# Kernel tuning notes

Measured on AMD Instinct MI355X. Metric: run time of the kernel, lower is better.

The kernel has to match this reference:

```python
import jax, jax.numpy as jnp
import numpy as np

TOL = 0.5          # Time_tolerance
DECAY = 1.0        # decay_rate
RES = 0.03         # integral_resolution
T_MAX = 120.0
G = 4000           # int(T_MAX / RES)


def setup_inputs() -> dict:
    key = jax.random.key(0)
    ks = jax.random.split(key, 8)
    B, N, H = 128, 64, 128
    times0 = jnp.sort(jax.random.uniform(ks[0], (B, N), dtype=jnp.float32) * T_MAX, axis=-1)
    times1 = jnp.sort(jax.random.uniform(ks[1], (B, N), dtype=jnp.float32) * T_MAX, axis=-1)
    states0 = jax.random.randint(ks[2], (B, N), 0, 2, dtype=jnp.int32)
    states1 = jax.random.randint(ks[3], (B, N), 0, 2, dtype=jnp.int32)
    head_times = jnp.sort(jax.random.uniform(ks[4], (B, H), dtype=jnp.float32) * T_MAX, axis=-1)
    head_states = jax.random.randint(ks[5], (B, H), 0, 2, dtype=jnp.int32)
    base = jnp.full((1,), -0.2, dtype=jnp.float32)  # torch.ones(1) * -0.2
    weights = jax.random.normal(ks[6], (2,), dtype=jnp.float32) * 0.1
    return dict(times0=times0, states0=states0, times1=times1, states1=states1,
                head_times=head_times, head_states=head_states, base=base, weights=weights)


def _intensity(t, times0, states0, times1, states1, head_times, head_states, base, wn):
    # t: [B,T] evaluation times; times*: [B,N]; head_*: [B,H]
    te = t[..., None]                                   # [B,T,1]
    t0 = times0[:, None, :]                             # [B,1,N]
    t1 = times1[:, None, :]
    s0 = states0[:, None, :]
    s1 = states1[:, None, :]
    # exp(-decay*(t - tau)); clamp dt>=0 so masked-out (future) events don't overflow
    dec0 = jnp.exp(-DECAY * jnp.maximum(te - t0, 0.0))  # [B,T,N]
    dec1 = jnp.exp(-DECAY * jnp.maximum(te - t1, 0.0))
    # Formula 0: body [0,1], signs [1,1], relations (0 BEFORE 1), (1 BEFORE head)
    A = jnp.where((t0 <= te) & (s0 == 1), dec0, 0.0)                 # history mask + kernel on pred0
    Bm = jnp.where((t1 < te - TOL) & (s1 == 1), dec1, 0.0)           # (t1 BEFORE head) + history mask
    M = (times0[:, :, None] - times1[:, None, :] < -TOL).astype(t.dtype)  # [B,N,N] (t0 BEFORE t1)
    feat0 = jnp.einsum('bti,bij,btj->bt', A, M, Bm)  # sum over itertools.product pairs
    # Formula 1: body [0], sign [0], relation (0 BEFORE head)
    feat1 = jnp.sum(jnp.where((t0 < te - TOL) & (s0 == 0), dec0, 0.0), axis=-1)
    # formula effect: cur_state via idx = sum(t > head_times) - 1 (numpy negative-index wrap)
    cnt = jnp.sum(te > head_times[:, None, :], axis=-1)              # [B,T]
    Hn = head_times.shape[-1]
    cur_state = jnp.take_along_axis(head_states, (cnt - 1) % Hn, axis=-1)
    eff0 = jnp.where(cur_state == 0, 1.0, -1.0).astype(t.dtype)      # head sign 1 -> +1 iff counter_state==1
    eff1 = -eff0                                                      # head sign 0
    return jnp.exp(base[0] + wn[0] * feat0 * eff0 + wn[1] * feat1 * eff1)


def reference(times0, states0, times1, states1, head_times, head_states, base, weights):
    wn = jax.nn.softmax(weights)  # exp(w)/sum exp(w)
    B = times0.shape[0]
    grid = jnp.broadcast_to((jnp.arange(G, dtype=times0.dtype) * RES)[None, :], (B, G))
    lam_grid = _intensity(grid, times0, states0, times1, states1, head_times, head_states, base, wn)
    lam_ev = _intensity(head_times[:, 1:], times0, states0, times1, states1, head_times, head_states, base, wn)
    log_sum = jnp.sum(jnp.log(lam_ev))
    integral = jnp.sum(lam_grid) * RES
    return (log_sum - integral).reshape(1)
```

## Files before the change

### kernel.cpp

```cpp
#include <hip/hip_runtime.h>
#include <math.h>

constexpr int Bb = 128;
constexpr int Nn = 64;
constexpr int Hh = 128;
constexpr int Gg = 4000;
constexpr float  TOLf = 0.5f;
constexpr double RESd = 0.03;

constexpr int GBLK  = 16;
constexpr int NGRID = Bb * GBLK;
constexpr int NBLK  = NGRID + Bb;
constexpr int TSTRIDE = 72;

__device__ __forceinline__ int lb64(const float* __restrict__ a, float key) {
    int lo = (a[31] < key) ? 32 : 0;
    lo += (a[lo + 15] < key) ? 16 : 0;
    lo += (a[lo + 7]  < key) ? 8  : 0;
    lo += (a[lo + 3]  < key) ? 4  : 0;
    lo += (a[lo + 1]  < key) ? 2  : 0;
    lo += (a[lo]      < key) ? 1  : 0;
    lo += (a[lo]      < key) ? 1  : 0;
    return lo;
}
__device__ __forceinline__ int ub64(const float* __restrict__ a, float key) {
    int lo = (a[31] <= key) ? 32 : 0;
    lo += (a[lo + 15] <= key) ? 16 : 0;
    lo += (a[lo + 7]  <= key) ? 8  : 0;
    lo += (a[lo + 3]  <= key) ? 4  : 0;
    lo += (a[lo + 1]  <= key) ? 2  : 0;
    lo += (a[lo]      <= key) ? 1  : 0;
    lo += (a[lo]      <= key) ? 1  : 0;
    return lo;
}
__device__ __forceinline__ int lb128(const float* __restrict__ a, float key) {
    int lo = (a[63] < key) ? 64 : 0;
    lo += (a[lo + 31] < key) ? 32 : 0;
    lo += (a[lo + 15] < key) ? 16 : 0;
    lo += (a[lo + 7]  < key) ? 8  : 0;
    lo += (a[lo + 3]  < key) ? 4  : 0;
    lo += (a[lo + 1]  < key) ? 2  : 0;
    lo += (a[lo]      < key) ? 1  : 0;
    lo += (a[lo]      < key) ? 1  : 0;
    return lo;
}

__global__ __launch_bounds__(64) void precompute_kernel(
    const float* __restrict__ times0, const int* __restrict__ states0,
    const float* __restrict__ times1, const int* __restrict__ states1,
    double* __restrict__ Ps_all, double* __restrict__ Qs_all,
    double* __restrict__ SW_all, double* __restrict__ SWP_all,
    int* __restrict__ kT_all)
{
    const int b = blockIdx.x;
    const int i = threadIdx.x;

    __shared__ float  t1s[Nn];
    __shared__ int    j0s[Nn];
    __shared__ double Ps_sh[Nn + 1];

    const float t0 = times0[b * Nn + i];
    const float t1 = times1[b * Nn + i];
    const int   s0 = states0[b * Nn + i];
    const int   s1 = states1[b * Nn + i];
    t1s[i] = t1;
    __syncthreads();

    int j0 = 0;
    #pragma unroll
    for (int j = 0; j < Nn; ++j)
        j0 += (t0 - t1s[j] >= -TOLf) ? 1 : 0;
    j0s[i] = j0;

    const double e0 = exp((double)t0);
    double vp = (s1 == 1) ? exp((double)t1) : 0.0;
    double vq = (s0 == 0) ? e0 : 0.0;
    const double W = (s0 == 1) ? e0 : 0.0;
    double vw = W;

    #pragma unroll
    for (int off = 1; off < 64; off <<= 1) {
        double op = __shfl_up(vp, off, 64);
        double oq = __shfl_up(vq, off, 64);
        double ow = __shfl_up(vw, off, 64);
        if (i >= off) { vp += op; vq += oq; vw += ow; }
    }
    Ps_sh[i + 1] = vp;
    if (i == 0) Ps_sh[0] = 0.0;
    __syncthreads();

    double vwp = W * Ps_sh[j0];
    #pragma unroll
    for (int off = 1; off < 64; off <<= 1) {
        double o = __shfl_up(vwp, off, 64);
        if (i >= off) vwp += o;
    }

    int kc = 0;
    #pragma unroll
    for (int j = 0; j < Nn; ++j)
        kc += (j0s[j] <= i) ? 1 : 0;

    double* Ps  = Ps_all  + b * TSTRIDE;
    double* Qs  = Qs_all  + b * TSTRIDE;
    double* SW  = SW_all  + b * TSTRIDE;
    double* SWP = SWP_all + b * TSTRIDE;
    int*    kT  = kT_all  + b * TSTRIDE;

    Ps[i + 1]  = vp;  Qs[i + 1]  = vq;
    SW[i + 1]  = vw;  SWP[i + 1] = vwp;
    kT[i] = kc;
    if (i == 0) {
        Ps[0] = 0.0; Qs[0] = 0.0; SW[0] = 0.0; SWP[0] = 0.0;
        kT[Nn] = Nn;
    }
}

__global__ __launch_bounds__(256) void eval_kernel(
    const float* __restrict__ times0, const float* __restrict__ times1,
    const float* __restrict__ head_times, const int* __restrict__ head_states,
    const float* __restrict__ base, const float* __restrict__ weights,
    const double* __restrict__ Ps_all, const double* __restrict__ Qs_all,
    const double* __restrict__ SW_all, const double* __restrict__ SWP_all,
    const int* __restrict__ kT_all,
    double* __restrict__ partials)
{
    __shared__ float  t0s[Nn], t1s[Nn];
    __shared__ float  hts[Hh];
    __shared__ int    hss[Hh];
    __shared__ double Ps[Nn + 1], Qs[Nn + 1], SW[Nn + 1], SWP[Nn + 1];
    __shared__ int    kT[Nn + 1];
    __shared__ double wsh[3];
    __shared__ double redsh[4];

    const int tid = threadIdx.x;
    const bool isEvent = blockIdx.x >= (unsigned)NGRID;
    const int b     = isEvent ? (blockIdx.x - NGRID) : (blockIdx.x >> 4);
    const int gbase = isEvent ? 0 : ((blockIdx.x & 15) << 8);
    const double tbase = (double)gbase * 0.03;

    if (tid < Nn) {
        t0s[tid] = times0[b * Nn + tid];
        t1s[tid] = times1[b * Nn + tid];
    } else if (tid < 192) {
        const int k = tid - 64;
        hts[k] = head_times[b * Hh + k];
        hss[k] = head_states[b * Hh + k];
    } else {
        const double sE = isEvent ? 1.0 : exp(-tbase);
        int k = tid - 192;
        const int base_i = b * TSTRIDE;
        Ps[k]  = Ps_all [base_i + k] * sE;
        Qs[k]  = Qs_all [base_i + k] * sE;
        SW[k]  = SW_all [base_i + k] * sE;
        SWP[k] = SWP_all[base_i + k] * (sE * sE);
        kT[k]  = kT_all [base_i + k];
        if (tid == 192) {
            k = Nn;
            Ps[k]  = Ps_all [base_i + k] * sE;
            Qs[k]  = Qs_all [base_i + k] * sE;
            SW[k]  = SW_all [base_i + k] * sE;
            SWP[k] = SWP_all[base_i + k] * (sE * sE);
            kT[k]  = kT_all [base_i + k];
        }
    }
    if (tid == 0) {
        const double w0 = (double)weights[0], w1 = (double)weights[1];
        const double mw = fmax(w0, w1);
        const double e0 = exp(w0 - mw), e1 = exp(w1 - mw);
        wsh[0] = e0 / (e0 + e1);
        wsh[1] = e1 / (e0 + e1);
        wsh[2] = (double)base[0];
    }
    __syncthreads();

    double contrib = 0.0;

    if (isEvent) {
        if (tid >= 1 && tid < Hh) {
            const float tf = hts[tid];
            const float thr = tf - TOLf;
            const int c   = lb64(t1s, thr);
            const int c0  = lb64(t0s, thr);
            const int c1  = ub64(t0s, tf);
            const int cnt = lb128(hts, tf);

            const int m = min(c1, kT[c]);
            const double a  = Ps[c] * SW[m] - SWP[m];
            const double ed = exp(-(double)tf);
            const double f0 = a * ed * ed;
            const double f1 = Qs[c0] * ed;
            const int cur = hss[((unsigned)(cnt - 1)) & (unsigned)(Hh - 1)];
            const double eff = (cur == 0) ? 1.0 : -1.0;
            contrib = wsh[2] + eff * (wsh[0] * f0 - wsh[1] * f1);
        }
    } else {
        const int g = gbase + tid;
        if (g < Gg) {
            const float tf = (float)g * 0.03f;
            const float thr = tf - TOLf;
            const int c   = lb64(t1s, thr);
            const int c0  = lb64(t0s, thr);
            const int c1  = ub64(t0s, tf);
            const int cnt = lb128(hts, tf);

            const int m = min(c1, kT[c]);
            const double a = Ps[c] * SW[m] - SWP[m];
            const double dt = (double)tf - tbase;
            const float f0 = (float)a * __expf((float)(-2.0 * dt));
            const float f1 = (float)Qs[c0] * __expf((float)(-dt));
            const int cur = hss[((unsigned)(cnt - 1)) & (unsigned)(Hh - 1)];
            const float eff = (cur == 0) ? 1.0f : -1.0f;
            const float ll = (float)wsh[2] + eff * ((float)wsh[0] * f0 - (float)wsh[1] * f1);
            contrib = -RESd * (double)__expf(ll);
        }
    }

    double v = contrib;
    #pragma unroll
    for (int off = 32; off > 0; off >>= 1) v += __shfl_down(v, off, 64);
    if ((tid & 63) == 0) redsh[tid >> 6] = v;
    __syncthreads();
    if (tid == 0) partials[blockIdx.x] = redsh[0] + redsh[1] + redsh[2] + redsh[3];
}

__global__ __launch_bounds__(256) void finalize_kernel(
    const double* __restrict__ partials, float* __restrict__ out)
{
    __shared__ double redsh[4];
    const int tid = threadIdx.x;
    double v = 0.0;
    for (int i = tid; i < NBLK; i += 256) v += partials[i];
    #pragma unroll
    for (int off = 32; off > 0; off >>= 1) v += __shfl_down(v, off, 64);
    if ((tid & 63) == 0) redsh[tid >> 6] = v;
    __syncthreads();
    if (tid == 0) out[0] = (float)(redsh[0] + redsh[1] + redsh[2] + redsh[3]);
}

extern "C" void kernel_launch(void* const* d_in, const int* in_sizes, int n_in,
                              void* d_out, int out_size, void* d_ws, size_t ws_size,
                              hipStream_t stream) {
    const float* times0      = (const float*)d_in[0];
    const int*   states0     = (const int*)  d_in[1];
    const float* times1      = (const float*)d_in[2];
    const int*   states1     = (const int*)  d_in[3];
    const float* head_times  = (const float*)d_in[4];
    const int*   head_states = (const int*)  d_in[5];
    const float* base        = (const float*)d_in[6];
    const float* weights     = (const float*)d_in[7];

    double* Ps_all  = (double*)d_ws;
    double* Qs_all  = Ps_all  + Bb * TSTRIDE;
    double* SW_all  = Qs_all  + Bb * TSTRIDE;
    double* SWP_all = SW_all  + Bb * TSTRIDE;
    int*    kT_all  = (int*)(SWP_all + Bb * TSTRIDE);
    double* partials = (double*)(kT_all + Bb * TSTRIDE);

    precompute_kernel<<<Bb, 64, 0, stream>>>(times0, states0, times1, states1,
                                             Ps_all, Qs_all, SW_all, SWP_all, kT_all);
    eval_kernel<<<NBLK, 256, 0, stream>>>(times0, times1, head_times, head_states,
                                          base, weights,
                                          Ps_all, Qs_all, SW_all, SWP_all, kT_all,
                                          partials);
    finalize_kernel<<<1, 256, 0, stream>>>(partials, (float*)d_out);
}
```

Measured before the change: 78.80 us.

## Precompute piecewise segment payloads so grid points use one merged-breakpoint search

The precompute kernel now merges all breakpoints per batch (shifted event thresholds and head times) into one sorted array of 512 entries. For each segment it stores a float4 payload with the pre-scaled feat0 and feat1 coefficients, sign and weights folded in. Each grid thread then does one 9-step binary search plus two exps instead of four binary searches and double-precision prefix-sum lookups. In exchange the precompute kernel does more serial work, and exact float threshold keys (thr_key via ulp stepping) are needed to keep the segment boundaries equivalent.

```diff
diff --git a/kernel.cpp b/kernel.cpp
--- a/kernel.cpp
+++ b/kernel.cpp
@@ -12,6 +12,11 @@
 constexpr int NGRID = Bb * GBLK;
 constexpr int NBLK  = NGRID + Bb;
 constexpr int TSTRIDE = 72;
+
+constexpr int NKEY = 3 * Nn + Hh;
+constexpr int BPS  = 512;
+constexpr int PAYS = 336;
+constexpr float BIGF = 1.0e30f;
 
 __device__ __forceinline__ int lb64(const float* __restrict__ a, float key) {
     int lo = (a[31] < key) ? 32 : 0;
@@ -44,76 +49,178 @@
     lo += (a[lo]      < key) ? 1  : 0;
     return lo;
 }
-
-__global__ __launch_bounds__(64) void precompute_kernel(
+__device__ __forceinline__ int lb512(const float* __restrict__ a, float key) {
+    int lo = (a[255] < key) ? 256 : 0;
+    lo += (a[lo + 127] < key) ? 128 : 0;
+    lo += (a[lo + 63]  < key) ? 64  : 0;
+    lo += (a[lo + 31]  < key) ? 32  : 0;
+    lo += (a[lo + 15]  < key) ? 16  : 0;
+    lo += (a[lo + 7]   < key) ? 8   : 0;
+    lo += (a[lo + 3]   < key) ? 4   : 0;
+    lo += (a[lo + 1]   < key) ? 2   : 0;
+    lo += (a[lo]       < key) ? 1   : 0;
+    return lo;
+}
+
+__device__ __forceinline__ float predf(float x) { return __uint_as_float(__float_as_uint(x) - 1u); }
+__device__ __forceinline__ float succf(float x) { return __uint_as_float(__float_as_uint(x) + 1u); }
+
+__device__ __forceinline__ float thr_key(float a) {
+    float v = a + 0.5f;
+    while (v - 0.5f <= a) v = succf(v);
+    while (v - 0.5f > a)  v = predf(v);
+    return v;
+}
+
+__global__ __launch_bounds__(320) void precompute_kernel(
     const float* __restrict__ times0, const int* __restrict__ states0,
     const float* __restrict__ times1, const int* __restrict__ states1,
+    const float* __restrict__ head_times, const int* __restrict__ head_states,
+    const float* __restrict__ base, const float* __restrict__ weights,
     double* __restrict__ Ps_all, double* __restrict__ Qs_all,
     double* __restrict__ SW_all, double* __restrict__ SWP_all,
-    int* __restrict__ kT_all)
+    int* __restrict__ kT_all,
+    float* __restrict__ bp_all, float4* __restrict__ pay_all)
 {
-    const int b = blockIdx.x;
-    const int i = threadIdx.x;
-
-    __shared__ float  t1s[Nn];
+    const int b   = blockIdx.x;
+    const int tid = threadIdx.x;
+
+    __shared__ float  t0s[Nn], t1s[Nn], hts[Hh];
+    __shared__ int    hss[Hh];
+    __shared__ float  k0[Nn], k1[Nn], k2[Nn];
+    __shared__ float  bp[BPS];
     __shared__ int    j0s[Nn];
-    __shared__ double Ps_sh[Nn + 1];
-
-    const float t0 = times0[b * Nn + i];
-    const float t1 = times1[b * Nn + i];
-    const int   s0 = states0[b * Nn + i];
-    const int   s1 = states1[b * Nn + i];
-    t1s[i] = t1;
-    __syncthreads();
-
-    int j0 = 0;
-    #pragma unroll
-    for (int j = 0; j < Nn; ++j)
-        j0 += (t0 - t1s[j] >= -TOLf) ? 1 : 0;
-    j0s[i] = j0;
-
-    const double e0 = exp((double)t0);
-    double vp = (s1 == 1) ? exp((double)t1) : 0.0;
-    double vq = (s0 == 0) ? e0 : 0.0;
-    const double W = (s0 == 1) ? e0 : 0.0;
-    double vw = W;
-
-    #pragma unroll
-    for (int off = 1; off < 64; off <<= 1) {
-        double op = __shfl_up(vp, off, 64);
-        double oq = __shfl_up(vq, off, 64);
-        double ow = __shfl_up(vw, off, 64);
-        if (i >= off) { vp += op; vq += oq; vw += ow; }
-    }
-    Ps_sh[i + 1] = vp;
-    if (i == 0) Ps_sh[0] = 0.0;
-    __syncthreads();
-
-    double vwp = W * Ps_sh[j0];
-    #pragma unroll
-    for (int off = 1; off < 64; off <<= 1) {
-        double o = __shfl_up(vwp, off, 64);
-        if (i >= off) vwp += o;
-    }
-
-    int kc = 0;
-    #pragma unroll
-    for (int j = 0; j < Nn; ++j)
-        kc += (j0s[j] <= i) ? 1 : 0;
-
-    double* Ps  = Ps_all  + b * TSTRIDE;
-    double* Qs  = Qs_all  + b * TSTRIDE;
-    double* SW  = SW_all  + b * TSTRIDE;
-    double* SWP = SWP_all + b * TSTRIDE;
-    int*    kT  = kT_all  + b * TSTRIDE;
-
-    Ps[i + 1]  = vp;  Qs[i + 1]  = vq;
-    SW[i + 1]  = vw;  SWP[i + 1] = vwp;
-    kT[i] = kc;
-    if (i == 0) {
-        Ps[0] = 0.0; Qs[0] = 0.0; SW[0] = 0.0; SWP[0] = 0.0;
-        kT[Nn] = Nn;
-    }
+    __shared__ double Ps[Nn + 1], Qs[Nn + 1], SW[Nn + 1], SWP[Nn + 1];
+    __shared__ int    kT[Nn + 1];
+    __shared__ double wsh2[2];
+
+    float t0 = 0.f, t1 = 0.f; int s0 = 0, s1 = 0;
+    double W = 0.0; int j0 = 0;
+
+    if (tid < Nn) {
+        t0 = times0[b * Nn + tid]; t1 = times1[b * Nn + tid];
+        s0 = states0[b * Nn + tid]; s1 = states1[b * Nn + tid];
+        t0s[tid] = t0; t1s[tid] = t1;
+    } else if (tid < 192) {
+        const int k = tid - 64;
+        hts[k] = head_times[b * Hh + k];
+        hss[k] = head_states[b * Hh + k];
+    } else if (tid == 192) {
+        const double w0 = (double)weights[0], w1 = (double)weights[1];
+        const double mw = fmax(w0, w1);
+        const double e0 = exp(w0 - mw), e1 = exp(w1 - mw);
+        wsh2[0] = e0 / (e0 + e1);
+        wsh2[1] = e1 / (e0 + e1);
+    }
+    __syncthreads();
+
+    if (tid < Nn) {
+        const int i = tid;
+        int c = 0;
+        #pragma unroll
+        for (int j = 0; j < Nn; ++j)
+            c += (t0 - t1s[j] >= -TOLf) ? 1 : 0;
+        j0 = c;
+        j0s[i] = c;
+        const double e0 = exp((double)t0);
+        double vp = (s1 == 1) ? exp((double)t1) : 0.0;
+        double vq = (s0 == 0) ? e0 : 0.0;
+        W = (s0 == 1) ? e0 : 0.0;
+        double vw = W;
+        #pragma unroll
+        for (int off = 1; off < 64; off <<= 1) {
+            double op = __shfl_up(vp, off, 64);
+            double oq = __shfl_up(vq, off, 64);
+            double ow = __shfl_up(vw, off, 64);
+            if (i >= off) { vp += op; vq += oq; vw += ow; }
+        }
+        Ps[i + 1] = vp; Qs[i + 1] = vq; SW[i + 1] = vw;
+        if (i == 0) { Ps[0] = 0.0; Qs[0] = 0.0; SW[0] = 0.0; SWP[0] = 0.0; }
+    } else if (tid < 128) {
+        const int j = tid - 64;
+        k0[j] = predf(thr_key(t1s[j]));
+    } else if (tid < 192) {
+        const int j = tid - 128;
+        k1[j] = predf(thr_key(t0s[j]));
+    } else if (tid < 256) {
+        const int j = tid - 192;
+        k2[j] = predf(t0s[j]);
+    } else {
+        for (int k = tid - 256; k < BPS - NKEY; k += 64)
+            bp[NKEY + k] = BIGF;
+    }
+    __syncthreads();
+
+    if (tid < Nn) {
+        const int i = tid;
+        double vwp = W * Ps[j0];
+        #pragma unroll
+        for (int off = 1; off < 64; off <<= 1) {
+            double o = __shfl_up(vwp, off, 64);
+            if (i >= off) vwp += o;
+        }
+        SWP[i + 1] = vwp;
+        int kc = 0;
+        #pragma unroll
+        for (int j = 0; j < Nn; ++j)
+            kc += (j0s[j] <= i) ? 1 : 0;
+        kT[i] = kc;
+        if (i == 0) kT[Nn] = Nn;
+
+        double* Psg  = Ps_all  + b * TSTRIDE;
+        double* Qsg  = Qs_all  + b * TSTRIDE;
+        double* SWg  = SW_all  + b * TSTRIDE;
+        double* SWPg = SWP_all + b * TSTRIDE;
+        int*    kTg  = kT_all  + b * TSTRIDE;
+        Psg[i + 1]  = Ps[i + 1];  Qsg[i + 1]  = Qs[i + 1];
+        SWg[i + 1]  = SW[i + 1];  SWPg[i + 1] = vwp;
+        kTg[i] = kc;
+        if (i == 0) {
+            Psg[0] = 0.0; Qsg[0] = 0.0; SWg[0] = 0.0; SWPg[0] = 0.0;
+            kTg[Nn] = Nn;
+        }
+    }
+    __syncthreads();
+
+    {
+        float myk; int rank;
+        if (tid < 64) {
+            myk = k0[tid];
+            rank = tid + lb64(k1, myk) + lb64(k2, myk) + lb128(hts, myk);
+        } else if (tid < 128) {
+            const int j = tid - 64; myk = k1[j];
+            rank = j + ub64(k0, myk) + lb64(k2, myk) + lb128(hts, myk);
+        } else if (tid < 192) {
+            const int j = tid - 128; myk = k2[j];
+            rank = j + ub64(k0, myk) + ub64(k1, myk) + lb128(hts, myk);
+        } else {
+            const int j = tid - 192; myk = hts[j];
+            rank = j + ub64(k0, myk) + ub64(k1, myk) + ub64(k2, myk);
+        }
+        bp[rank] = myk;
+    }
+    __syncthreads();
+
+    for (int s = tid; s <= NKEY; s += NKEY) {
+        const float t_rep = (s < NKEY) ? bp[s] : (BIGF * 2.0f);
+        const int c   = lb64(k0, t_rep);
+        const int c0  = lb64(k1, t_rep);
+        const int c1  = lb64(k2, t_rep);
+        const int cnt = lb128(hts, t_rep);
+        const int m = min(c1, kT[c]);
+        const double A = Ps[c] * SW[m] - SWP[m];
+        const double Q = Qs[c0];
+        const int cur = hss[((unsigned)(cnt - 1)) & (unsigned)(Hh - 1)];
+        const double eff = (cur == 0) ? 1.0 : -1.0;
+        const float  tsl = (s > 0) ? bp[s - 1] : 0.0f;
+        const double sE  = exp(-(double)tsl);
+        const float As = (float)(wsh2[0] * eff * A * (sE * sE));
+        const float Qv = (float)(wsh2[1] * eff * Q * sE);
+        pay_all[b * PAYS + s] = make_float4(As, Qv, tsl, 0.0f);
+        if (s >= NKEY) break;
+    }
+    for (int k = tid; k < BPS; k += 320)
+        bp_all[b * BPS + k] = bp[k];
 }
 
 __global__ __launch_bounds__(256) void eval_kernel(
@@ -123,6 +230,7 @@
     const double* __restrict__ Ps_all, const double* __restrict__ Qs_all,
     const double* __restrict__ SW_all, const double* __restrict__ SWP_all,
     const int* __restrict__ kT_all,
+    const float* __restrict__ bp_all, const float4* __restrict__ pay_all,
     double* __restrict__ partials)
 {
     __shared__ float  t0s[Nn], t1s[Nn];
@@ -132,45 +240,51 @@
     __shared__ int    kT[Nn + 1];
     __shared__ double wsh[3];
     __shared__ double redsh[4];
+    __shared__ float  bp[BPS];
+    __shared__ float4 pay[NKEY + 1];
+    __shared__ float  basef;
 
     const int tid = threadIdx.x;
     const bool isEvent = blockIdx.x >= (unsigned)NGRID;
-    const int b     = isEvent ? (blockIdx.x - NGRID) : (blockIdx.x >> 4);
-    const int gbase = isEvent ? 0 : ((blockIdx.x & 15) << 8);
-    const double tbase = (double)gbase * 0.03;
-
-    if (tid < Nn) {
-        t0s[tid] = times0[b * Nn + tid];
-        t1s[tid] = times1[b * Nn + tid];
-    } else if (tid < 192) {
-        const int k = tid - 64;
-        hts[k] = head_times[b * Hh + k];
-        hss[k] = head_states[b * Hh + k];
+    const int b = isEvent ? (blockIdx.x - NGRID) : (blockIdx.x >> 4);
+
+    if (isEvent) {
+        if (tid < Nn) {
+            t0s[tid] = times0[b * Nn + tid];
+            t1s[tid] = times1[b * Nn + tid];
+        } else if (tid < 192) {
+            const int k = tid - 64;
+            hts[k] = head_times[b * Hh + k];
+            hss[k] = head_states[b * Hh + k];
+        } else {
+            int k = tid - 192;
+            const int base_i = b * TSTRIDE;
+            Ps[k]  = Ps_all [base_i + k];
+            Qs[k]  = Qs_all [base_i + k];
+            SW[k]  = SW_all [base_i + k];
+            SWP[k] = SWP_all[base_i + k];
+            kT[k]  = kT_all [base_i + k];
+            if (tid == 192) {
+                k = Nn;
+                Ps[k]  = Ps_all [base_i + k];
+                Qs[k]  = Qs_all [base_i + k];
+                SW[k]  = SW_all [base_i + k];
+                SWP[k] = SWP_all[base_i + k];
+                kT[k]  = kT_all [base_i + k];
+            }
+        }
+        if (tid == 0) {
+            const double w0 = (double)weights[0], w1 = (double)weights[1];
+            const double mw = fmax(w0, w1);
+            const double e0 = exp(w0 - mw), e1 = exp(w1 - mw);
+            wsh[0] = e0 / (e0 + e1);
+            wsh[1] = e1 / (e0 + e1);
+            wsh[2] = (double)base[0];
+        }
     } else {
-        const double sE = isEvent ? 1.0 : exp(-tbase);
-        int k = tid - 192;
-        const int base_i = b * TSTRIDE;
-        Ps[k]  = Ps_all [base_i + k] * sE;
-        Qs[k]  = Qs_all [base_i + k] * sE;
-        SW[k]  = SW_all [base_i + k] * sE;
-        SWP[k] = SWP_all[base_i + k] * (sE * sE);
-        kT[k]  = kT_all [base_i + k];
-        if (tid == 192) {
-            k = Nn;
-            Ps[k]  = Ps_all [base_i + k] * sE;
-            Qs[k]  = Qs_all [base_i + k] * sE;
-            SW[k]  = SW_all [base_i + k] * sE;
-            SWP[k] = SWP_all[base_i + k] * (sE * sE);
-            kT[k]  = kT_all [base_i + k];
-        }
-    }
-    if (tid == 0) {
-        const double w0 = (double)weights[0], w1 = (double)weights[1];
-        const double mw = fmax(w0, w1);
-        const double e0 = exp(w0 - mw), e1 = exp(w1 - mw);
-        wsh[0] = e0 / (e0 + e1);
-        wsh[1] = e1 / (e0 + e1);
-        wsh[2] = (double)base[0];
+        for (int k = tid; k < BPS; k += 256) bp[k] = bp_all[b * BPS + k];
+        for (int k = tid; k < NKEY + 1; k += 256) pay[k] = pay_all[b * PAYS + k];
+        if (tid == 0) basef = base[0];
     }
     __syncthreads();
 
@@ -195,23 +309,13 @@
             contrib = wsh[2] + eff * (wsh[0] * f0 - wsh[1] * f1);
         }
     } else {
-        const int g = gbase + tid;
+        const int g = ((blockIdx.x & 15) << 8) + tid;
         if (g < Gg) {
             const float tf = (float)g * 0.03f;
-            const float thr = tf - TOLf;
-            const int c   = lb64(t1s, thr);
-            const int c0  = lb64(t0s, thr);
-            const int c1  = ub64(t0s, tf);
-            const int cnt = lb128(hts, tf);
-
-            const int m = min(c1, kT[c]);
-            const double a = Ps[c] * SW[m] - SWP[m];
-            const double dt = (double)tf - tbase;
-            const float f0 = (float)a * __expf((float)(-2.0 * dt));
-            const float f1 = (float)Qs[c0] * __expf((float)(-dt));
-            const int cur = hss[((unsigned)(cnt - 1)) & (unsigned)(Hh - 1)];
-            const float eff = (cur == 0) ? 1.0f : -1.0f;
-            const float ll = (float)wsh[2] + eff * ((float)wsh[0] * f0 - (float)wsh[1] * f1);
+            const int seg = lb512(bp, tf);
+            const float4 p = pay[seg];
+            const float ef = __expf(p.z - tf);
+            const float ll = basef + ef * fmaf(ef, p.x, -p.y);
             contrib = -RESd * (double)__expf(ll);
         }
     }
@@ -256,12 +360,17 @@
     double* SWP_all = SW_all  + Bb * TSTRIDE;
     int*    kT_all  = (int*)(SWP_all + Bb * TSTRIDE);
     double* partials = (double*)(kT_all + Bb * TSTRIDE);
-
-    precompute_kernel<<<Bb, 64, 0, stream>>>(times0, states0, times1, states1,
-                                             Ps_all, Qs_all, SW_all, SWP_all, kT_all);
+    float*  bp_all   = (float*)(partials + NBLK);
+    float4* pay_all  = (float4*)(bp_all + Bb * BPS);
+
+    precompute_kernel<<<Bb, 320, 0, stream>>>(times0, states0, times1, states1,
+                                              head_times, head_states, base, weights,
+                                              Ps_all, Qs_all, SW_all, SWP_all, kT_all,
+                                              bp_all, pay_all);
     eval_kernel<<<NBLK, 256, 0, stream>>>(times0, times1, head_times, head_states,
                                           base, weights,
                                           Ps_all, Qs_all, SW_all, SWP_all, kT_all,
+                                          bp_all, pay_all,
                                           partials);
     finalize_kernel<<<1, 256, 0, stream>>>(partials, (float*)d_out);
 }
```

Result: slower. 81.27 us (+3.1%).
